# Performance work log

Hardware: AMD Instinct MI355X
Metric: run time of the kernel (lower is better)

## Reference

```python
import jax, jax.numpy as jnp
import numpy as np
import math

B, S, H, D = 4, 4096, 2048, 128  # batch, seq_len, hidden_dim, head_size

def setup_inputs() -> dict:
    key = jax.random.key(0)
    ks = jax.random.split(key, 7)
    scale = 1.0 / math.sqrt(H)
    return {
        "x": jax.random.normal(ks[0], (B, S, H), dtype=jnp.float32),
        "Wq": jax.random.normal(ks[1], (H, D), dtype=jnp.float32) * scale,
        "bq": jnp.zeros((D,), dtype=jnp.float32),
        "Wk": jax.random.normal(ks[2], (H, D), dtype=jnp.float32) * scale,
        "bk": jnp.zeros((D,), dtype=jnp.float32),
        "Wv": jax.random.normal(ks[3], (H, D), dtype=jnp.float32) * scale,
        "bv": jnp.zeros((D,), dtype=jnp.float32),
    }

def reference(x, Wq, bq, Wk, bk, Wv, bv):
    # projections: [B,S,D]
    q = x @ Wq + bq
    k = x @ Wk + bk
    v = x @ Wv + bv
    # raw scores [B,S,S] with causal mask, NO pre-softmax scaling (as in source)
    scores = jnp.einsum('bsd,btd->bst', q, k)
    causal = jnp.tril(jnp.ones((S, S), dtype=bool))
    scores = jnp.where(causal, scores, -jnp.inf)
    # non-standard: scale AFTER softmax by 1/sqrt(head_size)
    w = jax.nn.softmax(scores, axis=-1) * (1.0 / math.sqrt(D))
    # dropout p=0.0 -> identity
    return jnp.einsum('bst,btd->bsd', w, v)
```

## Files before the change

kernel.cpp:

```cpp
#include <hip/hip_runtime.h>
#include <math.h>
#include <stdint.h>

#define SEQ   4096
#define HID   2048
#define HD    128
#define NROWS 16384

typedef __attribute__((ext_vector_type(8))) short bf16x8;
typedef __attribute__((ext_vector_type(4))) float f32x4;

static constexpr float OSCALE = 0.088388347648318447f;

using gvptr = const __attribute__((address_space(1))) void*;
using lvptr = __attribute__((address_space(3))) void*;
__device__ __forceinline__ void gld_lds16(const void* g, void* l) {
    __builtin_amdgcn_global_load_lds((gvptr)g, (lvptr)l, 16, 0, 0);
}

__device__ __forceinline__ unsigned short f2bf_rne(float f) {
    union { float f; unsigned u; } v; v.f = f;
    unsigned u = v.u + 0x7fffu + ((v.u >> 16) & 1u);
    return (unsigned short)(u >> 16);
}
__device__ __forceinline__ unsigned short f2bf_tr(float f) {
    union { float f; unsigned u; } v; v.f = f;
    return (unsigned short)(v.u >> 16);
}
__device__ __forceinline__ float bf2f(unsigned short h) {
    union { unsigned u; float f; } v; v.u = ((unsigned)h) << 16;
    return v.f;
}

__global__ __launch_bounds__(256) void prep_w(
    const float* __restrict__ Wq, const float* __restrict__ Wk, const float* __restrict__ Wv,
    unsigned short* __restrict__ wth, unsigned short* __restrict__ wtl)
{
    __shared__ float T[64][68];
    const int tid = threadIdx.x;
    const int k0 = blockIdx.x * 64, n0 = blockIdx.y * 64, mm = blockIdx.z;
    const float* W = (mm == 0) ? Wq : (mm == 1) ? Wk : Wv;
    #pragma unroll
    for (int i = 0; i < 4; ++i) {
        const int fi = i * 256 + tid, kk = fi >> 4, nc = (fi & 15) * 4;
        const float4 w = *(const float4*)(W + (size_t)(k0 + kk) * HD + n0 + nc);
        T[kk][nc] = w.x; T[kk][nc + 1] = w.y; T[kk][nc + 2] = w.z; T[kk][nc + 3] = w.w;
    }
    __syncthreads();
    unsigned short* oh = wth + (size_t)mm * HD * HID;
    unsigned short* ol = wtl + (size_t)mm * HD * HID;
    #pragma unroll
    for (int i = 0; i < 4; ++i) {
        const int fi = i * 256 + tid, nn = fi >> 4, kc = (fi & 15) * 4;
        const float a = T[kc][nn], b = T[kc + 1][nn], c = T[kc + 2][nn], d = T[kc + 3][nn];
        ushort4 hv, lv;
        hv.x = f2bf_rne(a); hv.y = f2bf_rne(b); hv.z = f2bf_rne(c); hv.w = f2bf_rne(d);
        lv.x = f2bf_rne(a - bf2f(hv.x)); lv.y = f2bf_rne(b - bf2f(hv.y));
        lv.z = f2bf_rne(c - bf2f(hv.z)); lv.w = f2bf_rne(d - bf2f(hv.w));
        *(ushort4*)(oh + (size_t)(n0 + nn) * HID + k0 + kc) = hv;
        *(ushort4*)(ol + (size_t)(n0 + nn) * HID + k0 + kc) = lv;
    }
}

__global__ __launch_bounds__(256, 3) void qkv_split(
    const float* __restrict__ x,
    const float* __restrict__ bq, const float* __restrict__ bk, const float* __restrict__ bv,
    const unsigned short* __restrict__ wth, const unsigned short* __restrict__ wtl,
    unsigned short* __restrict__ qh, unsigned short* __restrict__ ql,
    unsigned short* __restrict__ kh, unsigned short* __restrict__ kl,
    unsigned short* __restrict__ vth)
{
    __shared__ unsigned short Ah[64][64], Al[64][64];
    __shared__ unsigned short Bh[128][64], Bl[128][64];

    const int tid = threadIdx.x, wave = tid >> 6, lane = tid & 63;
    const int l15 = lane & 15, q4 = lane >> 4;
    const int wr = wave >> 1, wc = wave & 1;
    const int type = blockIdx.x % 3;
    const int tile = blockIdx.x / 3;
    const int r0 = tile * 64;
    const bool qk = (type < 2);

    const unsigned short* wh = wth + (size_t)type * HD * HID;
    const unsigned short* wl = wtl + (size_t)type * HD * HID;

    const int srow   = lane >> 3;
    const int schunk = ((lane & 7) ^ srow) * 8;

    f32x4 acc[2][4];
    #pragma unroll
    for (int mt = 0; mt < 2; ++mt)
        #pragma unroll
        for (int nt = 0; nt < 4; ++nt)
            acc[mt][nt] = (f32x4){0.f, 0.f, 0.f, 0.f};

    const float* xbase = x + (size_t)r0 * HID;

    float4 xv[4];
    #pragma unroll
    for (int i = 0; i < 4; ++i) {
        const int fi = i * 256 + tid, row = fi >> 4, kc = (fi & 15) * 4;
        xv[i] = *(const float4*)(xbase + (size_t)row * HID + kc);
    }

    for (int k0 = 0; k0 < HID; k0 += 64) {
        __syncthreads();

        {
            #pragma unroll
            for (int c = 0; c < 4; ++c) {
                const int row = wave * 32 + c * 8;
                gld_lds16(wh + (size_t)(row + srow) * HID + k0 + schunk, &Bh[row][0]);
            }
            if (qk) {
                #pragma unroll
                for (int c = 0; c < 4; ++c) {
                    const int row = wave * 32 + c * 8;
                    gld_lds16(wl + (size_t)(row + srow) * HID + k0 + schunk, &Bl[row][0]);
                }
            }
        }
        #pragma unroll
        for (int i = 0; i < 4; ++i) {
            const int fi = i * 256 + tid, row = fi >> 4, kc = (fi & 15) * 4;
            const int pk = ((kc >> 3) ^ (row & 7)) * 8 + (kc & 7);
            ushort4 hv;
            hv.x = f2bf_tr(xv[i].x); hv.y = f2bf_tr(xv[i].y);
            hv.z = f2bf_tr(xv[i].z); hv.w = f2bf_tr(xv[i].w);
            *(ushort4*)&Ah[row][pk] = hv;
            if (qk) {
                ushort4 lv;
                lv.x = f2bf_tr(xv[i].x - bf2f(hv.x)); lv.y = f2bf_tr(xv[i].y - bf2f(hv.y));
                lv.z = f2bf_tr(xv[i].z - bf2f(hv.z)); lv.w = f2bf_tr(xv[i].w - bf2f(hv.w));
                *(ushort4*)&Al[row][pk] = lv;
            }
        }
        __syncthreads();

        const int kn = (k0 + 64 < HID) ? (k0 + 64) : 0;
        #pragma unroll
        for (int i = 0; i < 4; ++i) {
            const int fi = i * 256 + tid, row = fi >> 4, kc = (fi & 15) * 4;
            xv[i] = *(const float4*)(xbase + (size_t)row * HID + kn + kc);
        }

        #pragma unroll
        for (int ks = 0; ks < 2; ++ks) {
            const int pc = ((ks * 4 + q4) ^ (l15 & 7)) * 8;
            bf16x8 ah[2], al[2];
            #pragma unroll
            for (int mt = 0; mt < 2; ++mt) {
                const int ar = wr * 32 + mt * 16 + l15;
                ah[mt] = *(const bf16x8*)&Ah[ar][pc];
                if (qk) al[mt] = *(const bf16x8*)&Al[ar][pc];
            }
            #pragma unroll
            for (int nt = 0; nt < 4; ++nt) {
                const int br = wc * 64 + nt * 16 + l15;
                const bf16x8 bh = *(const bf16x8*)&Bh[br][pc];
                #pragma unroll
                for (int mt = 0; mt < 2; ++mt)
                    acc[mt][nt] = __builtin_amdgcn_mfma_f32_16x16x32_bf16(ah[mt], bh, acc[mt][nt], 0, 0, 0);
                if (qk) {
                    const bf16x8 bl = *(const bf16x8*)&Bl[br][pc];
                    #pragma unroll
                    for (int mt = 0; mt < 2; ++mt) {
                        acc[mt][nt] = __builtin_amdgcn_mfma_f32_16x16x32_bf16(ah[mt], bl, acc[mt][nt], 0, 0, 0);
                        acc[mt][nt] = __builtin_amdgcn_mfma_f32_16x16x32_bf16(al[mt], bh, acc[mt][nt], 0, 0, 0);
                    }
                }
            }
        }
    }

    if (qk) {
        const float* bb = (type == 0) ? bq : bk;
        unsigned short* oh = (type == 0) ? qh : kh;
        unsigned short* ol = (type == 0) ? ql : kl;
        #pragma unroll
        for (int nt = 0; nt < 4; ++nt) {
            const int col = wc * 64 + nt * 16 + l15;
            const float bias = bb[col];
            #pragma unroll
            for (int mt = 0; mt < 2; ++mt) {
                const int Rb = r0 + wr * 32 + mt * 16 + q4 * 4;
                #pragma unroll
                for (int r = 0; r < 4; ++r) {
                    const float v = acc[mt][nt][r] + bias;
                    const unsigned short h = f2bf_rne(v);
                    oh[(size_t)(Rb + r) * HD + col] = h;
                    ol[(size_t)(Rb + r) * HD + col] = f2bf_rne(v - bf2f(h));
                }
            }
        }
    } else {
        #pragma unroll
        for (int nt = 0; nt < 4; ++nt) {
            const int col = wc * 64 + nt * 16 + l15;
            const float bias = bv[col];
            #pragma unroll
            for (int mt = 0; mt < 2; ++mt) {
                const int Rb = r0 + wr * 32 + mt * 16 + q4 * 4;
                const int bi = Rb >> 12, s0 = Rb & 4095;
                ushort4 pv;
                pv.x = f2bf_rne(acc[mt][nt][0] + bias);
                pv.y = f2bf_rne(acc[mt][nt][1] + bias);
                pv.z = f2bf_rne(acc[mt][nt][2] + bias);
                pv.w = f2bf_rne(acc[mt][nt][3] + bias);
                *(ushort4*)(vth + ((size_t)(bi * HD + col)) * SEQ + s0) = pv;
            }
        }
    }
}

__global__ __launch_bounds__(256, 2) void flash_mfma(
    const unsigned short* __restrict__ qh, const unsigned short* __restrict__ ql,
    const unsigned short* __restrict__ kh, const unsigned short* __restrict__ kl,
    const unsigned short* __restrict__ vth,
    unsigned short* __restrict__ oPb, float* __restrict__ mP, float* __restrict__ lP)
{
    __shared__ unsigned short Kh[64][128], Kl[64][128];
    __shared__ unsigned short Vt[128][64];
    __shared__ unsigned short Ps[4][16][72];

    const int tid = threadIdx.x, wave = tid >> 6, lane = tid & 63;
    const int l15 = lane & 15, q4 = lane >> 4;
    const int h = blockIdx.x & 3, pair = (blockIdx.x >> 2) & 31, b = blockIdx.x >> 7;

    const int krow_l = lane >> 4;
    const int vrow_l = lane >> 3;
    const int vsc = ((lane & 7) ^ (vrow_l & 7)) * 8;
    const int kkey7 = l15 & 7;
    const int vkey7 = l15 & 7;

    for (int side = 0; side < 2; ++side) {
        const int tt = side ? (63 - pair) : pair;
        const int n = tt + 1;
        const int j0 = (n * h) >> 2, j1 = (n * (h + 1)) >> 2;

        const int qrow = b * SEQ + tt * 64 + wave * 16 + l15;
        bf16x8 aqh[4], aql[4];
        #pragma unroll
        for (int ks = 0; ks < 4; ++ks) {
            aqh[ks] = *(const bf16x8*)(qh + (size_t)qrow * HD + ks * 32 + q4 * 8);
            aql[ks] = *(const bf16x8*)(ql + (size_t)qrow * HD + ks * 32 + q4 * 8);
        }
        f32x4 oa[8];
        #pragma unroll
        for (int d = 0; d < 8; ++d) oa[d] = (f32x4){0.f, 0.f, 0.f, 0.f};
        float m_r = -INFINITY;
        float l_r = 0.f;

        for (int j = j0; j < j1; ++j) {
            __syncthreads();
            {
                const size_t kb = (size_t)b * SEQ + j * 64;
                #pragma unroll
                for (int c = 0; c < 4; ++c) {
                    const int rl = c * 4 + krow_l;
                    const int sc = (l15 ^ (rl & 7)) * 8;
                    const size_t gr = (kb + wave * 16 + rl) * HD + sc;
                    gld_lds16(kh + gr, &Kh[wave * 16 + c * 4][0]);
                    gld_lds16(kl + gr, &Kl[wave * 16 + c * 4][0]);
                }
                #pragma unroll
                for (int c = 0; c < 4; ++c)
                    gld_lds16(vth + ((size_t)(b * HD + wave * 32 + c * 8 + vrow_l)) * SEQ
                                  + j * 64 + vsc,
                              &Vt[wave * 32 + c * 8][0]);
            }
            __syncthreads();

            f32x4 s[4];
            #pragma unroll
            for (int nt = 0; nt < 4; ++nt) s[nt] = (f32x4){0.f, 0.f, 0.f, 0.f};
            __builtin_amdgcn_s_setprio(1);
            #pragma unroll
            for (int ks = 0; ks < 4; ++ks) {
                const int pc = ((ks * 4 + q4) ^ kkey7) * 8;
                #pragma unroll
                for (int nt = 0; nt < 4; ++nt) {
                    const bf16x8 bh = *(const bf16x8*)&Kh[nt * 16 + l15][pc];
                    const bf16x8 bl = *(const bf16x8*)&Kl[nt * 16 + l15][pc];
                    s[nt] = __builtin_amdgcn_mfma_f32_16x16x32_bf16(bh, aqh[ks], s[nt], 0, 0, 0);
                    s[nt] = __builtin_amdgcn_mfma_f32_16x16x32_bf16(bh, aql[ks], s[nt], 0, 0, 0);
                    s[nt] = __builtin_amdgcn_mfma_f32_16x16x32_bf16(bl, aqh[ks], s[nt], 0, 0, 0);
                }
            }
            __builtin_amdgcn_s_setprio(0);

            if (j == tt) {
                const int qloc = wave * 16 + l15;
                #pragma unroll
                for (int nt = 0; nt < 4; ++nt)
                    #pragma unroll
                    for (int r = 0; r < 4; ++r) {
                        const int kvl = nt * 16 + q4 * 4 + r;
                        if (kvl > qloc) s[nt][r] = -INFINITY;
                    }
            }

            float mt = fmaxf(fmaxf(s[0][0], s[0][1]), fmaxf(s[0][2], s[0][3]));
            #pragma unroll
            for (int nt = 1; nt < 4; ++nt)
                mt = fmaxf(mt, fmaxf(fmaxf(s[nt][0], s[nt][1]), fmaxf(s[nt][2], s[nt][3])));
            mt = fmaxf(mt, __shfl_xor(mt, 16));
            mt = fmaxf(mt, __shfl_xor(mt, 32));

            const bool allskip = __all(mt <= m_r + 8.f);
            const float mn = allskip ? m_r : fmaxf(m_r, mt);

            f32x4 pf[4];
            #pragma unroll
            for (int nt = 0; nt < 4; ++nt)
                #pragma unroll
                for (int r = 0; r < 4; ++r)
                    pf[nt][r] = __expf(s[nt][r] - mn);

            #pragma unroll
            for (int nt = 0; nt < 4; ++nt) {
                ushort4 w;
                w.x = f2bf_tr(pf[nt][0]); w.y = f2bf_tr(pf[nt][1]);
                w.z = f2bf_tr(pf[nt][2]); w.w = f2bf_tr(pf[nt][3]);
                *(ushort4*)&Ps[wave][l15][nt * 16 + q4 * 4] = w;
            }

            float ps = ((pf[0][0] + pf[0][1]) + (pf[0][2] + pf[0][3]))
                     + ((pf[1][0] + pf[1][1]) + (pf[1][2] + pf[1][3]))
                     + ((pf[2][0] + pf[2][1]) + (pf[2][2] + pf[2][3]))
                     + ((pf[3][0] + pf[3][1]) + (pf[3][2] + pf[3][3]));
            ps += __shfl_xor(ps, 16);
            ps += __shfl_xor(ps, 32);

            if (allskip) {
                l_r += ps;
            } else {
                const float al = __expf(m_r - mn);
                m_r = mn;
                l_r = l_r * al + ps;
                #pragma unroll
                for (int r = 0; r < 4; ++r) {
                    const float alr = __shfl(al, (q4 << 2) | r);
                    #pragma unroll
                    for (int d = 0; d < 8; ++d) oa[d][r] *= alr;
                }
            }

            const bf16x8 ap0 = *(const bf16x8*)&Ps[wave][l15][q4 * 8];
            const bf16x8 ap1 = *(const bf16x8*)&Ps[wave][l15][32 + q4 * 8];
            __builtin_amdgcn_s_setprio(1);
            #pragma unroll
            for (int d = 0; d < 8; ++d) {
                const bf16x8 bv0 = *(const bf16x8*)&Vt[d * 16 + l15][(q4 ^ vkey7) * 8];
                const bf16x8 bv1 = *(const bf16x8*)&Vt[d * 16 + l15][((4 + q4) ^ vkey7) * 8];
                oa[d] = __builtin_amdgcn_mfma_f32_16x16x32_bf16(ap0, bv0, oa[d], 0, 0, 0);
                oa[d] = __builtin_amdgcn_mfma_f32_16x16x32_bf16(ap1, bv1, oa[d], 0, 0, 0);
            }
            __builtin_amdgcn_s_setprio(0);
        }

        const int R0 = b * SEQ + tt * 64 + wave * 16 + q4 * 4;
        unsigned short* op = oPb + (size_t)h * NROWS * HD;
        #pragma unroll
        for (int d = 0; d < 8; ++d)
            #pragma unroll
            for (int r = 0; r < 4; ++r)
                op[(size_t)(R0 + r) * HD + d * 16 + l15] = f2bf_rne(oa[d][r]);
        if (q4 == 0) {
            const int qr = b * SEQ + tt * 64 + wave * 16 + l15;
            mP[h * NROWS + qr] = m_r;
            lP[h * NROWS + qr] = l_r;
        }
    }
}

__global__ __launch_bounds__(256) void flash_merge(
    const unsigned short* __restrict__ oPb, const float* __restrict__ mP,
    const float* __restrict__ lP, float* __restrict__ out)
{
    const int idx = blockIdx.x * 256 + threadIdx.x;
    const int r = idx >> 5, c = (idx & 31) * 4;
    float m[4], l[4];
    #pragma unroll
    for (int i = 0; i < 4; ++i) { m[i] = mP[i * NROWS + r]; l[i] = lP[i * NROWS + r]; }
    float M = fmaxf(fmaxf(m[0], m[1]), fmaxf(m[2], m[3]));
    float a[4], lsum = 0.f;
    #pragma unroll
    for (int i = 0; i < 4; ++i) { a[i] = __expf(m[i] - M); lsum += l[i] * a[i]; }
    const float inv = OSCALE / lsum;
    float ox = 0.f, oy = 0.f, oz = 0.f, ow = 0.f;
    #pragma unroll
    for (int i = 0; i < 4; ++i) {
        const ushort4 ov = *(const ushort4*)(oPb + (size_t)i * NROWS * HD + (size_t)r * HD + c);
        ox += a[i] * bf2f(ov.x); oy += a[i] * bf2f(ov.y);
        oz += a[i] * bf2f(ov.z); ow += a[i] * bf2f(ov.w);
    }
    float4 o; o.x = ox * inv; o.y = oy * inv; o.z = oz * inv; o.w = ow * inv;
    *(float4*)(out + (size_t)r * HD + c) = o;
}

extern "C" void kernel_launch(void* const* d_in, const int* in_sizes, int n_in,
                              void* d_out, int out_size, void* d_ws, size_t ws_size,
                              hipStream_t stream)
{
    (void)in_sizes; (void)n_in; (void)out_size; (void)ws_size;
    const float* x  = (const float*)d_in[0];
    const float* Wq = (const float*)d_in[1];
    const float* bq = (const float*)d_in[2];
    const float* Wk = (const float*)d_in[3];
    const float* bk = (const float*)d_in[4];
    const float* Wv = (const float*)d_in[5];
    const float* bv = (const float*)d_in[6];
    float* out = (float*)d_out;

    char* w = (char*)d_ws;
    unsigned short* qh  = (unsigned short*)(w);
    unsigned short* ql  = (unsigned short*)(w + 4194304);
    unsigned short* kh  = (unsigned short*)(w + 8388608);
    unsigned short* kl  = (unsigned short*)(w + 12582912);
    unsigned short* vth = (unsigned short*)(w + 16777216);
    unsigned short* wth = (unsigned short*)(w + 20971520);
    unsigned short* wtl = (unsigned short*)(w + 22544384);
    unsigned short* oPb = (unsigned short*)(w + 24117248);
    float* mP = (float*)(w + 40894464);
    float* lP = (float*)(w + 41156608);

    prep_w<<<dim3(32, 2, 3), 256, 0, stream>>>(Wq, Wk, Wv, wth, wtl);
    qkv_split<<<768, 256, 0, stream>>>(x, bq, bk, bv, wth, wtl, qh, ql, kh, kl, vth);
    flash_mfma<<<512, 256, 0, stream>>>(qh, ql, kh, kl, vth, oPb, mP, lP);
    flash_merge<<<2048, 256, 0, stream>>>(oPb, mP, lP, out);
}
```

Measured before the change: 304.0 us.

## Drop paired-tile loop, launch one block per tile, pass P via shuffles

```diff
diff --git a/kernel.cpp b/kernel.cpp
--- a/kernel.cpp
+++ b/kernel.cpp
@@ -213,7 +213,7 @@
     }
 }
 
-__global__ __launch_bounds__(256, 2) void flash_mfma(
+__global__ __launch_bounds__(256, 3) void flash_mfma(
     const unsigned short* __restrict__ qh, const unsigned short* __restrict__ ql,
     const unsigned short* __restrict__ kh, const unsigned short* __restrict__ kl,
     const unsigned short* __restrict__ vth,
@@ -221,11 +221,13 @@
 {
     __shared__ unsigned short Kh[64][128], Kl[64][128];
     __shared__ unsigned short Vt[128][64];
-    __shared__ unsigned short Ps[4][16][72];
 
     const int tid = threadIdx.x, wave = tid >> 6, lane = tid & 63;
     const int l15 = lane & 15, q4 = lane >> 4;
-    const int h = blockIdx.x & 3, pair = (blockIdx.x >> 2) & 31, b = blockIdx.x >> 7;
+    const int b = blockIdx.x & 3, h = (blockIdx.x >> 2) & 3, tord = blockIdx.x >> 4;
+    const int tt = 63 - tord;
+    const int n = tt + 1;
+    const int j0 = (n * h) >> 2, j1 = (n * (h + 1)) >> 2;
 
     const int krow_l = lane >> 4;
     const int vrow_l = lane >> 3;
@@ -233,144 +235,162 @@
     const int kkey7 = l15 & 7;
     const int vkey7 = l15 & 7;
 
-    for (int side = 0; side < 2; ++side) {
-        const int tt = side ? (63 - pair) : pair;
-        const int n = tt + 1;
-        const int j0 = (n * h) >> 2, j1 = (n * (h + 1)) >> 2;
-
-        const int qrow = b * SEQ + tt * 64 + wave * 16 + l15;
-        bf16x8 aqh[4], aql[4];
+    const int qrow = b * SEQ + tt * 64 + wave * 16 + l15;
+    bf16x8 aqh[4], aql[4];
+    #pragma unroll
+    for (int ks = 0; ks < 4; ++ks) {
+        aqh[ks] = *(const bf16x8*)(qh + (size_t)qrow * HD + ks * 32 + q4 * 8);
+        aql[ks] = *(const bf16x8*)(ql + (size_t)qrow * HD + ks * 32 + q4 * 8);
+    }
+    f32x4 oa[8];
+    #pragma unroll
+    for (int d = 0; d < 8; ++d) oa[d] = (f32x4){0.f, 0.f, 0.f, 0.f};
+    float m_r = -INFINITY;
+    float l_r = 0.f;
+
+    for (int j = j0; j < j1; ++j) {
+        __syncthreads();
+        {
+            const size_t kb = (size_t)b * SEQ + j * 64;
+            #pragma unroll
+            for (int c = 0; c < 4; ++c) {
+                const int rl = c * 4 + krow_l;
+                const int sc = (l15 ^ (rl & 7)) * 8;
+                const size_t gr = (kb + wave * 16 + rl) * HD + sc;
+                gld_lds16(kh + gr, &Kh[wave * 16 + c * 4][0]);
+                gld_lds16(kl + gr, &Kl[wave * 16 + c * 4][0]);
+            }
+            #pragma unroll
+            for (int c = 0; c < 4; ++c)
+                gld_lds16(vth + ((size_t)(b * HD + wave * 32 + c * 8 + vrow_l)) * SEQ
+                              + j * 64 + vsc,
+                          &Vt[wave * 32 + c * 8][0]);
+        }
+        __syncthreads();
+
+        f32x4 s[4];
+        #pragma unroll
+        for (int nt = 0; nt < 4; ++nt) s[nt] = (f32x4){0.f, 0.f, 0.f, 0.f};
+        __builtin_amdgcn_s_setprio(1);
         #pragma unroll
         for (int ks = 0; ks < 4; ++ks) {
-            aqh[ks] = *(const bf16x8*)(qh + (size_t)qrow * HD + ks * 32 + q4 * 8);
-            aql[ks] = *(const bf16x8*)(ql + (size_t)qrow * HD + ks * 32 + q4 * 8);
-        }
-        f32x4 oa[8];
-        #pragma unroll
-        for (int d = 0; d < 8; ++d) oa[d] = (f32x4){0.f, 0.f, 0.f, 0.f};
-        float m_r = -INFINITY;
-        float l_r = 0.f;
-
-        for (int j = j0; j < j1; ++j) {
-            __syncthreads();
-            {
-                const size_t kb = (size_t)b * SEQ + j * 64;
-                #pragma unroll
-                for (int c = 0; c < 4; ++c) {
-                    const int rl = c * 4 + krow_l;
-                    const int sc = (l15 ^ (rl & 7)) * 8;
-                    const size_t gr = (kb + wave * 16 + rl) * HD + sc;
-                    gld_lds16(kh + gr, &Kh[wave * 16 + c * 4][0]);
-                    gld_lds16(kl + gr, &Kl[wave * 16 + c * 4][0]);
-                }
-                #pragma unroll
-                for (int c = 0; c < 4; ++c)
-                    gld_lds16(vth + ((size_t)(b * HD + wave * 32 + c * 8 + vrow_l)) * SEQ
-                                  + j * 64 + vsc,
-                              &Vt[wave * 32 + c * 8][0]);
-            }
-            __syncthreads();
-
-            f32x4 s[4];
-            #pragma unroll
-            for (int nt = 0; nt < 4; ++nt) s[nt] = (f32x4){0.f, 0.f, 0.f, 0.f};
-            __builtin_amdgcn_s_setprio(1);
-            #pragma unroll
-            for (int ks = 0; ks < 4; ++ks) {
-                const int pc = ((ks * 4 + q4) ^ kkey7) * 8;
-                #pragma unroll
-                for (int nt = 0; nt < 4; ++nt) {
-                    const bf16x8 bh = *(const bf16x8*)&Kh[nt * 16 + l15][pc];
-                    const bf16x8 bl = *(const bf16x8*)&Kl[nt * 16 + l15][pc];
-                    s[nt] = __builtin_amdgcn_mfma_f32_16x16x32_bf16(bh, aqh[ks], s[nt], 0, 0, 0);
-                    s[nt] = __builtin_amdgcn_mfma_f32_16x16x32_bf16(bh, aql[ks], s[nt], 0, 0, 0);
-                    s[nt] = __builtin_amdgcn_mfma_f32_16x16x32_bf16(bl, aqh[ks], s[nt], 0, 0, 0);
-                }
-            }
-            __builtin_amdgcn_s_setprio(0);
-
-            if (j == tt) {
-                const int qloc = wave * 16 + l15;
-                #pragma unroll
-                for (int nt = 0; nt < 4; ++nt)
-                    #pragma unroll
-                    for (int r = 0; r < 4; ++r) {
-                        const int kvl = nt * 16 + q4 * 4 + r;
-                        if (kvl > qloc) s[nt][r] = -INFINITY;
-                    }
-            }
-
-            float mt = fmaxf(fmaxf(s[0][0], s[0][1]), fmaxf(s[0][2], s[0][3]));
-            #pragma unroll
-            for (int nt = 1; nt < 4; ++nt)
-                mt = fmaxf(mt, fmaxf(fmaxf(s[nt][0], s[nt][1]), fmaxf(s[nt][2], s[nt][3])));
-            mt = fmaxf(mt, __shfl_xor(mt, 16));
-            mt = fmaxf(mt, __shfl_xor(mt, 32));
-
-            const bool allskip = __all(mt <= m_r + 8.f);
-            const float mn = allskip ? m_r : fmaxf(m_r, mt);
-
-            f32x4 pf[4];
+            const int pc = ((ks * 4 + q4) ^ kkey7) * 8;
+            #pragma unroll
+            for (int nt = 0; nt < 4; ++nt) {
+                const bf16x8 bh = *(const bf16x8*)&Kh[nt * 16 + l15][pc];
+                const bf16x8 bl = *(const bf16x8*)&Kl[nt * 16 + l15][pc];
+                s[nt] = __builtin_amdgcn_mfma_f32_16x16x32_bf16(bh, aqh[ks], s[nt], 0, 0, 0);
+                s[nt] = __builtin_amdgcn_mfma_f32_16x16x32_bf16(bh, aql[ks], s[nt], 0, 0, 0);
+                s[nt] = __builtin_amdgcn_mfma_f32_16x16x32_bf16(bl, aqh[ks], s[nt], 0, 0, 0);
+            }
+        }
+        __builtin_amdgcn_s_setprio(0);
+
+        if (j == tt) {
+            const int qloc = wave * 16 + l15;
             #pragma unroll
             for (int nt = 0; nt < 4; ++nt)
                 #pragma unroll
-                for (int r = 0; r < 4; ++r)
-                    pf[nt][r] = __expf(s[nt][r] - mn);
-
-            #pragma unroll
-            for (int nt = 0; nt < 4; ++nt) {
-                ushort4 w;
-                w.x = f2bf_tr(pf[nt][0]); w.y = f2bf_tr(pf[nt][1]);
-                w.z = f2bf_tr(pf[nt][2]); w.w = f2bf_tr(pf[nt][3]);
-                *(ushort4*)&Ps[wave][l15][nt * 16 + q4 * 4] = w;
-            }
-
-            float ps = ((pf[0][0] + pf[0][1]) + (pf[0][2] + pf[0][3]))
-                     + ((pf[1][0] + pf[1][1]) + (pf[1][2] + pf[1][3]))
-                     + ((pf[2][0] + pf[2][1]) + (pf[2][2] + pf[2][3]))
-                     + ((pf[3][0] + pf[3][1]) + (pf[3][2] + pf[3][3]));
-            ps += __shfl_xor(ps, 16);
-            ps += __shfl_xor(ps, 32);
-
-            if (allskip) {
-                l_r += ps;
-            } else {
-                const float al = __expf(m_r - mn);
-                m_r = mn;
-                l_r = l_r * al + ps;
+                for (int r = 0; r < 4; ++r) {
+                    const int kvl = nt * 16 + q4 * 4 + r;
+                    if (kvl > qloc) s[nt][r] = -INFINITY;
+                }
+        }
+
+        float mt = fmaxf(fmaxf(s[0][0], s[0][1]), fmaxf(s[0][2], s[0][3]));
+        #pragma unroll
+        for (int nt = 1; nt < 4; ++nt)
+            mt = fmaxf(mt, fmaxf(fmaxf(s[nt][0], s[nt][1]), fmaxf(s[nt][2], s[nt][3])));
+        mt = fmaxf(mt, __shfl_xor(mt, 16));
+        mt = fmaxf(mt, __shfl_xor(mt, 32));
+
+        const bool allskip = __all(mt <= m_r + 8.f);
+        const float mn = allskip ? m_r : fmaxf(m_r, mt);
+
+        f32x4 pf[4];
+        #pragma unroll
+        for (int nt = 0; nt < 4; ++nt)
+            #pragma unroll
+            for (int r = 0; r < 4; ++r)
+                pf[nt][r] = __expf(s[nt][r] - mn);
+
+        float ps = ((pf[0][0] + pf[0][1]) + (pf[0][2] + pf[0][3]))
+                 + ((pf[1][0] + pf[1][1]) + (pf[1][2] + pf[1][3]))
+                 + ((pf[2][0] + pf[2][1]) + (pf[2][2] + pf[2][3]))
+                 + ((pf[3][0] + pf[3][1]) + (pf[3][2] + pf[3][3]));
+        ps += __shfl_xor(ps, 16);
+        ps += __shfl_xor(ps, 32);
+
+        if (allskip) {
+            l_r += ps;
+        } else {
+            const float al = __expf(m_r - mn);
+            m_r = mn;
+            l_r = l_r * al + ps;
+            #pragma unroll
+            for (int r = 0; r < 4; ++r) {
+                const float alr = __shfl(al, (q4 << 2) | r);
                 #pragma unroll
-                for (int r = 0; r < 4; ++r) {
-                    const float alr = __shfl(al, (q4 << 2) | r);
-                    #pragma unroll
-                    for (int d = 0; d < 8; ++d) oa[d][r] *= alr;
-                }
-            }
-
-            const bf16x8 ap0 = *(const bf16x8*)&Ps[wave][l15][q4 * 8];
-            const bf16x8 ap1 = *(const bf16x8*)&Ps[wave][l15][32 + q4 * 8];
-            __builtin_amdgcn_s_setprio(1);
-            #pragma unroll
-            for (int d = 0; d < 8; ++d) {
-                const bf16x8 bv0 = *(const bf16x8*)&Vt[d * 16 + l15][(q4 ^ vkey7) * 8];
-                const bf16x8 bv1 = *(const bf16x8*)&Vt[d * 16 + l15][((4 + q4) ^ vkey7) * 8];
-                oa[d] = __builtin_amdgcn_mfma_f32_16x16x32_bf16(ap0, bv0, oa[d], 0, 0, 0);
-                oa[d] = __builtin_amdgcn_mfma_f32_16x16x32_bf16(ap1, bv1, oa[d], 0, 0, 0);
-            }
-            __builtin_amdgcn_s_setprio(0);
-        }
-
-        const int R0 = b * SEQ + tt * 64 + wave * 16 + q4 * 4;
-        unsigned short* op = oPb + (size_t)h * NROWS * HD;
-        #pragma unroll
-        for (int d = 0; d < 8; ++d)
-            #pragma unroll
-            for (int r = 0; r < 4; ++r)
-                op[(size_t)(R0 + r) * HD + d * 16 + l15] = f2bf_rne(oa[d][r]);
-        if (q4 == 0) {
-            const int qr = b * SEQ + tt * 64 + wave * 16 + l15;
-            mP[h * NROWS + qr] = m_r;
-            lP[h * NROWS + qr] = l_r;
-        }
+                for (int d = 0; d < 8; ++d) oa[d][r] *= alr;
+            }
+        }
+
+        unsigned cc[4][2];
+        #pragma unroll
+        for (int nt = 0; nt < 4; ++nt) {
+            cc[nt][0] = (unsigned)f2bf_tr(pf[nt][0]) | ((unsigned)f2bf_tr(pf[nt][1]) << 16);
+            cc[nt][1] = (unsigned)f2bf_tr(pf[nt][2]) | ((unsigned)f2bf_tr(pf[nt][3]) << 16);
+        }
+        unsigned t0[2], t1[2], t2[2], t3[2];
+        #pragma unroll
+        for (int d = 0; d < 2; ++d) {
+            t0[d] = (unsigned)__shfl_xor((int)cc[0][d], 16);
+            t1[d] = (unsigned)__shfl_xor((int)cc[1][d], 16);
+            t2[d] = (unsigned)__shfl_xor((int)cc[2][d], 16);
+            t3[d] = (unsigned)__shfl_xor((int)cc[3][d], 16);
+        }
+        const bool ev = (q4 & 1) == 0;
+        unsigned X0[2], X1[2], X2[2], X3[2];
+        #pragma unroll
+        for (int d = 0; d < 2; ++d) {
+            X0[d] = ev ? cc[0][d] : t1[d];
+            X1[d] = ev ? t0[d] : cc[1][d];
+            X2[d] = ev ? cc[2][d] : t3[d];
+            X3[d] = ev ? t2[d] : cc[3][d];
+        }
+        const int srcl = ((((q4 & 1) << 1) | (q4 >> 1)) << 4) | l15;
+        union { unsigned u[4]; bf16x8 v; } A0, A1;
+        A0.u[0] = (unsigned)__shfl((int)X0[0], srcl);
+        A0.u[1] = (unsigned)__shfl((int)X0[1], srcl);
+        A0.u[2] = (unsigned)__shfl((int)X1[0], srcl);
+        A0.u[3] = (unsigned)__shfl((int)X1[1], srcl);
+        A1.u[0] = (unsigned)__shfl((int)X2[0], srcl);
+        A1.u[1] = (unsigned)__shfl((int)X2[1], srcl);
+        A1.u[2] = (unsigned)__shfl((int)X3[0], srcl);
+        A1.u[3] = (unsigned)__shfl((int)X3[1], srcl);
+
+        __builtin_amdgcn_s_setprio(1);
+        #pragma unroll
+        for (int d = 0; d < 8; ++d) {
+            const bf16x8 bv0 = *(const bf16x8*)&Vt[d * 16 + l15][(q4 ^ vkey7) * 8];
+            const bf16x8 bv1 = *(const bf16x8*)&Vt[d * 16 + l15][((4 + q4) ^ vkey7) * 8];
+            oa[d] = __builtin_amdgcn_mfma_f32_16x16x32_bf16(A0.v, bv0, oa[d], 0, 0, 0);
+            oa[d] = __builtin_amdgcn_mfma_f32_16x16x32_bf16(A1.v, bv1, oa[d], 0, 0, 0);
+        }
+        __builtin_amdgcn_s_setprio(0);
+    }
+
+    const int R0 = b * SEQ + tt * 64 + wave * 16 + q4 * 4;
+    unsigned short* op = oPb + (size_t)h * NROWS * HD;
+    #pragma unroll
+    for (int d = 0; d < 8; ++d)
+        #pragma unroll
+        for (int r = 0; r < 4; ++r)
+            op[(size_t)(R0 + r) * HD + d * 16 + l15] = f2bf_rne(oa[d][r]);
+    if (q4 == 0) {
+        const int qr = b * SEQ + tt * 64 + wave * 16 + l15;
+        mP[h * NROWS + qr] = m_r;
+        lP[h * NROWS + qr] = l_r;
     }
 }
 
@@ -427,6 +447,6 @@
 
     prep_w<<<dim3(32, 2, 3), 256, 0, stream>>>(Wq, Wk, Wv, wth, wtl);
     qkv_split<<<768, 256, 0, stream>>>(x, bq, bk, bv, wth, wtl, qh, ql, kh, kl, vth);
-    flash_mfma<<<512, 256, 0, stream>>>(qh, ql, kh, kl, vth, oPb, mP, lP);
+    flash_mfma<<<1024, 256, 0, stream>>>(qh, ql, kh, kl, vth, oPb, mP, lP);
     flash_merge<<<2048, 256, 0, stream>>>(oPb, mP, lP, out);
 }
```

Result: no change. 303.5 us (-0.2%).
